# Kernel tuning notes

Hardware: AMD Instinct MI355X
Metric: run time of the kernel (lower is better)

The kernel has to match this reference:

```python
import jax, jax.numpy as jnp
import numpy as np

N_NODES = 50000
N_EDGES = 800000
IN_CH = 128
OUT_CH = 64


def setup_inputs() -> dict:
    key = jax.random.key(0)
    ks = jax.random.split(key, 8)
    cat = IN_CH + OUT_CH
    scale = 1.0 / np.sqrt(cat)
    return {
        "x": jax.random.normal(ks[0], (N_NODES, IN_CH), dtype=jnp.float32),
        "edge_index": jax.random.randint(ks[1], (2, N_EDGES), 0, N_NODES, dtype=jnp.int64),
        "edge_weight": jax.random.uniform(ks[2], (N_EDGES,), dtype=jnp.float32),
        "hidden_state": jax.random.normal(ks[3], (N_NODES, OUT_CH), dtype=jnp.float32),
        "W_z": jax.random.normal(ks[4], (cat, OUT_CH), dtype=jnp.float32) * scale,
        "b_z": jnp.zeros((OUT_CH,), dtype=jnp.float32),
        "W_r": jax.random.normal(ks[5], (cat, OUT_CH), dtype=jnp.float32) * scale,
        "b_r": jnp.zeros((OUT_CH,), dtype=jnp.float32),
        "W_h": jax.random.normal(ks[6], (cat, OUT_CH), dtype=jnp.float32) * scale,
        "b_h": jnp.zeros((OUT_CH,), dtype=jnp.float32),
    }


def _gcn_norm(row, col, w, num_nodes):
    # PyG GCNConv normalization with self-loops (fill_value=1):
    # norm_e = deg[row]^-1/2 * w_e * deg[col]^-1/2 over loop-augmented edges
    loops = jnp.arange(num_nodes, dtype=row.dtype)
    row = jnp.concatenate([row, loops])
    col = jnp.concatenate([col, loops])
    w = jnp.concatenate([w, jnp.ones((num_nodes,), dtype=w.dtype)])
    deg = jax.ops.segment_sum(w, col, num_segments=num_nodes)
    dinv = jnp.where(deg > 0, jax.lax.rsqrt(deg), 0.0)
    norm = dinv[row] * w * dinv[col]
    return row, col, norm


def _gcn_conv(x_cat, W, b, row, col, norm, num_nodes):
    h = x_cat @ W                                   # (N, out)
    msg = h[row] * norm[:, None]                    # (E+N, out) gather + scale
    out = jax.ops.segment_sum(msg, col, num_segments=num_nodes)
    return out + b


def reference(x, edge_index, edge_weight, hidden_state,
              W_z, b_z, W_r, b_r, W_h, b_h):
    n = x.shape[0]
    row, col, norm = _gcn_norm(edge_index[0], edge_index[1], edge_weight, n)
    xh = jnp.concatenate([x, hidden_state], axis=1)
    z = jax.nn.sigmoid(_gcn_conv(xh, W_z, b_z, row, col, norm, n))
    r = jax.nn.sigmoid(_gcn_conv(xh, W_r, b_r, row, col, norm, n))
    xrh = jnp.concatenate([x, r * hidden_state], axis=1)
    h_cand = jnp.tanh(_gcn_conv(xrh, W_h, b_h, row, col, norm, n))
    return z * hidden_state + (1.0 - z) * h_cand
```

## Files before the change

kernel.cpp:

```cpp
#include <hip/hip_runtime.h>
#include <hip/hip_bf16.h>
#include <cstdint>
#include <cstddef>

#define IN_CH   128
#define OUT_CH  64
#define CAT_CH  192

typedef short bf16x8 __attribute__((ext_vector_type(8)));
typedef float f32x4  __attribute__((ext_vector_type(4)));
typedef float f32x2  __attribute__((ext_vector_type(2)));
typedef unsigned long long u64;
typedef unsigned int u32;

__device__ __forceinline__ float sigmoidf_(float x) { return 1.f / (1.f + __expf(-x)); }

__device__ __forceinline__ unsigned short f2bf(float f) {
    u32 u = __float_as_uint(f);
    u32 r = (u + 0x7fffu + ((u >> 16) & 1u)) >> 16;
    return (unsigned short)r;
}
__device__ __forceinline__ float bflo(u32 v) { return __uint_as_float(v << 16); }
__device__ __forceinline__ float bfhi(u32 v) { return __uint_as_float(v & 0xffff0000u); }

__device__ __forceinline__ unsigned char f2e4m3(float f) {
    u32 p = __builtin_amdgcn_cvt_pk_fp8_f32(f, f, 0, false);
    return (unsigned char)p;
}
template <bool HI>
__device__ __forceinline__ f32x2 fp8pk(u32 v) {
    return __builtin_amdgcn_cvt_pk_f32_fp8((int)v, HI);
}

__global__ void detect_kernel(const unsigned int* __restrict__ ei, int* __restrict__ flag) {
    unsigned int v = ei[(threadIdx.x << 1) + 1];
    unsigned long long b = __ballot(v != 0u);
    if (threadIdx.x == 0) *flag = (b != 0ull) ? 1 : 0;
}

__device__ __forceinline__ int load_col(const void* ei, int i, int E, int f) {
    return f ? ((const int*)ei)[E + i] : (int)((const long long*)ei)[E + i];
}
__device__ __forceinline__ int load_row(const void* ei, int i, int E, int f) {
    return f ? ((const int*)ei)[i] : (int)((const long long*)ei)[i];
}

__global__ void hist2_kernel(const void* __restrict__ ei, const float* __restrict__ w,
                             u64* __restrict__ packed8, u32* __restrict__ rank,
                             const int* __restrict__ flag, int E, int N) {
    int i0 = (blockIdx.x * blockDim.x + threadIdx.x) * 2;
    if (i0 >= E) return;
    const u32 shard = blockIdx.x & 7;
    u64* __restrict__ shp = packed8 + (size_t)shard * N;
    int f = *flag;
    u32 rk[2];
#pragma unroll
    for (int k = 0; k < 2; k++) {
        int i = i0 + k;
        if (i < E) {
            int c = load_col(ei, i, E, f);
            u32 wq = __float2uint_rn(w[i] * 1048576.0f);
            u64 old = atomicAdd(&shp[c], (1ull << 32) | (u64)wq);
            rk[k] = (shard << 28) | (u32)(old >> 32);
        }
    }
#pragma unroll
    for (int k = 0; k < 2; k++)
        if (i0 + k < E) rank[i0 + k] = rk[k];
}

__global__ __launch_bounds__(256) void scan1_kernel(const u64* __restrict__ packed8,
                                                    float* __restrict__ dinv,
                                                    u32* __restrict__ shoff,
                                                    int* __restrict__ starts,
                                                    int* __restrict__ bsum, int n) {
    __shared__ int s[256];
    int i = blockIdx.x * 256 + threadIdx.x;
    int v = 0;
    if (i < n) {
        u32 run = 0, wsum = 0;
#pragma unroll
        for (int sh = 0; sh < 8; sh++) {
            u64 p = packed8[(size_t)sh * n + i];
            shoff[(size_t)sh * n + i] = run;
            run  += (u32)(p >> 32);
            wsum += (u32)p;
        }
        float ws = (float)wsum * (1.0f / 1048576.0f);
        dinv[i] = rsqrtf(1.0f + ws);
        v = (int)run;
    }
    s[threadIdx.x] = v;
    __syncthreads();
#pragma unroll
    for (int d = 1; d < 256; d <<= 1) {
        int t = (threadIdx.x >= d) ? s[threadIdx.x - d] : 0;
        __syncthreads();
        s[threadIdx.x] += t;
        __syncthreads();
    }
    if (i < n) starts[i] = s[threadIdx.x] - v;
    if (threadIdx.x == 255) bsum[blockIdx.x] = s[255];
}

__global__ __launch_bounds__(256) void scan2_kernel(int* __restrict__ bsum, int nb) {
    __shared__ int s[256];
    int t = threadIdx.x;
    int v = (t < nb) ? bsum[t] : 0;
    s[t] = v;
    __syncthreads();
#pragma unroll
    for (int d = 1; d < 256; d <<= 1) {
        int u = (t >= d) ? s[t - d] : 0;
        __syncthreads();
        s[t] += u;
        __syncthreads();
    }
    if (t < nb) bsum[t] = s[t] - v;
}

__global__ void scan3_kernel(int* __restrict__ starts, const int* __restrict__ boff,
                             int n, int E) {
    int i = blockIdx.x * blockDim.x + threadIdx.x;
    if (i == 0) starts[n] = E;
    if (i < n) starts[i] += boff[blockIdx.x];
}

__global__ void scatter2_kernel(const void* __restrict__ ei, const float* __restrict__ w,
                                const float* __restrict__ dinv, const int* __restrict__ starts,
                                const u32* __restrict__ shoff, const u32* __restrict__ rank,
                                u64* __restrict__ pairs, const int* __restrict__ flag,
                                int E, int N) {
    int i0 = (blockIdx.x * blockDim.x + threadIdx.x) * 4;
    if (i0 >= E) return;
    int f = *flag;
    int r[4], c[4];
#pragma unroll
    for (int k = 0; k < 4; k++) {
        int i = i0 + k;
        if (i < E) { r[k] = load_row(ei, i, E, f); c[k] = load_col(ei, i, E, f); }
    }
#pragma unroll
    for (int k = 0; k < 4; k++) {
        int i = i0 + k;
        if (i < E) {
            float nm = dinv[r[k]] * w[i] * dinv[c[k]];
            u32 rk = rank[i];
            u32 sh = rk >> 28, rks = rk & 0x0fffffffu;
            int pos = starts[c[k]] + (int)shoff[(size_t)sh * N + c[k]] + (int)rks;
            pairs[pos] = ((u64)__float_as_uint(nm) << 32) | (u32)(r[k] << 7);
        }
    }
}

__global__ void cvt_kernel(const float* __restrict__ x, const float* __restrict__ hidden,
                           unsigned short* __restrict__ xb, unsigned short* __restrict__ hb,
                           int nx, int nh) {
    int i4 = (blockIdx.x * blockDim.x + threadIdx.x) * 4;
    if (i4 < nx) {
        float4 v = *(const float4*)&x[i4];
        ushort4 o = { f2bf(v.x), f2bf(v.y), f2bf(v.z), f2bf(v.w) };
        *(ushort4*)&xb[i4] = o;
    } else {
        int j = i4 - nx;
        if (j < nh) {
            float4 v = *(const float4*)&hidden[j];
            ushort4 o = { f2bf(v.x), f2bf(v.y), f2bf(v.z), f2bf(v.w) };
            *(ushort4*)&hb[j] = o;
        }
    }
}

__global__ void packW_kernel(const float* __restrict__ Wz, const float* __restrict__ Wr,
                             const float* __restrict__ Wh,
                             unsigned short* __restrict__ Bzrt, unsigned short* __restrict__ Wht) {
    int i = blockIdx.x * blockDim.x + threadIdx.x;
    if (i >= 192 * CAT_CH) return;
    int col = i / CAT_CH, k = i % CAT_CH;
    if (col < 128) {
        float v = (col < 64) ? Wz[k * 64 + col] : Wr[k * 64 + (col - 64)];
        Bzrt[col * CAT_CH + k] = f2bf(v);
    } else {
        Wht[(col - 128) * CAT_CH + k] = f2bf(Wh[k * 64 + (col - 128)]);
    }
}

template <int TN, bool FP8OUT>
__global__ __launch_bounds__(256) void gemm_bf16_kernel(
    const unsigned short* __restrict__ A0, int a0w,
    const unsigned short* __restrict__ A1, int a1w,
    const unsigned short* __restrict__ Bt,
    void* __restrict__ Cout, int nrows)
{
    __shared__ unsigned short As[128][48];
    __shared__ unsigned short Bs[TN][200];

    const int t = threadIdx.x, lane = t & 63, wave = t >> 6;
    const int rowBase = blockIdx.x * 128;

    for (int idx = t * 8; idx < TN * CAT_CH; idx += 256 * 8) {
        int col = idx / CAT_CH, k = idx % CAT_CH;
        *(int4*)&Bs[col][k] = *(const int4*)&Bt[idx];
    }

    f32x4 acc[2][TN / 16];
#pragma unroll
    for (int rf = 0; rf < 2; rf++)
#pragma unroll
        for (int cf = 0; cf < TN / 16; cf++) acc[rf][cf] = (f32x4){0.f, 0.f, 0.f, 0.f};

    const int srow = t >> 1, half = t & 1;
    int arow = rowBase + srow;
    if (arow >= nrows) arow = nrows - 1;

    for (int k0 = 0; k0 < CAT_CH; k0 += 32) {
        __syncthreads();
        {
            const unsigned short* src = (k0 < a0w)
                ? A0 + (size_t)arow * a0w + k0
                : A1 + (size_t)arow * a1w + (k0 - a0w);
            *(int4*)&As[srow][half * 16] = *(const int4*)(src + half * 16);
            *(int4*)&As[srow][half * 16 + 8] = *(const int4*)(src + half * 16 + 8);
        }
        __syncthreads();

        const int rbase = wave * 32;
        const int koff = (lane >> 4) * 8;
        bf16x8 a0 = *(const bf16x8*)&As[rbase + (lane & 15)][koff];
        bf16x8 a1 = *(const bf16x8*)&As[rbase + 16 + (lane & 15)][koff];
#pragma unroll
        for (int cf = 0; cf < TN / 16; cf++) {
            bf16x8 b = *(const bf16x8*)&Bs[cf * 16 + (lane & 15)][k0 + koff];
            acc[0][cf] = __builtin_amdgcn_mfma_f32_16x16x32_bf16(a0, b, acc[0][cf], 0, 0, 0);
            acc[1][cf] = __builtin_amdgcn_mfma_f32_16x16x32_bf16(a1, b, acc[1][cf], 0, 0, 0);
        }
    }

#pragma unroll
    for (int rf = 0; rf < 2; rf++)
#pragma unroll
        for (int cf = 0; cf < TN / 16; cf++) {
            int row0 = rowBase + wave * 32 + rf * 16 + (lane >> 4) * 4;
            int col  = cf * 16 + (lane & 15);
#pragma unroll
            for (int r = 0; r < 4; r++) {
                int row = row0 + r;
                if (row < nrows) {
                    if (FP8OUT)
                        ((unsigned char*)Cout)[(size_t)row * TN + col] = f2e4m3(acc[rf][cf][r]);
                    else
                        ((unsigned short*)Cout)[(size_t)row * TN + col] = f2bf(acc[rf][cf][r]);
                }
            }
        }
}

__global__ __launch_bounds__(256) void spmm_zr_kernel(
    const unsigned char* __restrict__ H8, const u64* __restrict__ pairs,
    const int* __restrict__ starts, const float* __restrict__ dinv,
    const float* __restrict__ hidden, const float* __restrict__ bz,
    const float* __restrict__ br, float* __restrict__ Z,
    unsigned short* __restrict__ RHb, int N)
{
    int node = (blockIdx.x * 256 + threadIdx.x) >> 6;
    if (node >= N) return;
    const int lane = threadIdx.x & 63;
    const int sub = lane & 31, half = lane >> 5;
    int s = starts[node], e = starts[node + 1];
    float d = dinv[node], d2 = d * d;

    float a0 = 0.f, a1 = 0.f, a2 = 0.f, a3 = 0.f;
    if (half == 0) {
        u32 sv = *(const u32*)&H8[(size_t)node * 128 + sub * 4];
        f32x2 s01 = fp8pk<false>(sv), s23 = fp8pk<true>(sv);
        a0 = s01.x * d2; a1 = s01.y * d2; a2 = s23.x * d2; a3 = s23.y * d2;
    }

    int j = s;
    int full = s + ((e - s) & ~15);
    for (; j < full; j += 16) {
        u32 hv[8]; float nm[8];
#pragma unroll
        for (int k = 0; k < 8; k++) {
            u64 p = pairs[j + k * 2 + half];
            nm[k] = __uint_as_float((u32)(p >> 32));
            hv[k] = *(const u32*)&H8[(size_t)(u32)p + sub * 4];
        }
#pragma unroll
        for (int k = 0; k < 8; k++) {
            f32x2 h01 = fp8pk<false>(hv[k]), h23 = fp8pk<true>(hv[k]);
            a0 = fmaf(h01.x, nm[k], a0); a1 = fmaf(h01.y, nm[k], a1);
            a2 = fmaf(h23.x, nm[k], a2); a3 = fmaf(h23.y, nm[k], a3);
        }
    }
    if (j < e) {
        u32 hv[8]; float nm[8];
#pragma unroll
        for (int k = 0; k < 8; k++) {
            int jj = j + k * 2 + half;
            u64 p = pairs[(jj < e) ? jj : (e - 1)];
            nm[k] = (jj < e) ? __uint_as_float((u32)(p >> 32)) : 0.f;
            hv[k] = *(const u32*)&H8[(size_t)(u32)p + sub * 4];
        }
#pragma unroll
        for (int k = 0; k < 8; k++) {
            f32x2 h01 = fp8pk<false>(hv[k]), h23 = fp8pk<true>(hv[k]);
            a0 = fmaf(h01.x, nm[k], a0); a1 = fmaf(h01.y, nm[k], a1);
            a2 = fmaf(h23.x, nm[k], a2); a3 = fmaf(h23.y, nm[k], a3);
        }
    }

    a0 += __shfl_xor(a0, 32, 64);
    a1 += __shfl_xor(a1, 32, 64);
    a2 += __shfl_xor(a2, 32, 64);
    a3 += __shfl_xor(a3, 32, 64);

    if (half == 0) {
        if (sub < 16) {
            int c = sub * 4;
            float4 b4 = *(const float4*)&bz[c];
            float4 o = { sigmoidf_(a0 + b4.x), sigmoidf_(a1 + b4.y),
                         sigmoidf_(a2 + b4.z), sigmoidf_(a3 + b4.w) };
            *(float4*)&Z[(size_t)node * 64 + c] = o;
        } else {
            int c = (sub - 16) * 4;
            float4 b4 = *(const float4*)&br[c];
            float4 hid = *(const float4*)&hidden[(size_t)node * 64 + c];
            float r0 = sigmoidf_(a0 + b4.x) * hid.x;
            float r1 = sigmoidf_(a1 + b4.y) * hid.y;
            float r2 = sigmoidf_(a2 + b4.z) * hid.z;
            float r3 = sigmoidf_(a3 + b4.w) * hid.w;
            ushort4 o = { f2bf(r0), f2bf(r1), f2bf(r2), f2bf(r3) };
            *(ushort4*)&RHb[(size_t)node * 64 + c] = o;
        }
    }
}

__global__ __launch_bounds__(256) void spmm_h_kernel(
    const unsigned short* __restrict__ H, const u64* __restrict__ pairs,
    const int* __restrict__ starts, const float* __restrict__ dinv,
    const float* __restrict__ hidden, const float* __restrict__ bh,
    const float* __restrict__ Z, float* __restrict__ out, int N)
{
    int node = (blockIdx.x * 256 + threadIdx.x) >> 6;
    if (node >= N) return;
    const int lane = threadIdx.x & 63;
    const int sub = lane & 31, half = lane >> 5;
    const unsigned char* Hb = (const unsigned char*)H;
    int s = starts[node], e = starts[node + 1];
    float d = dinv[node], d2 = d * d;

    float ax = 0.f, ay = 0.f;
    if (half == 0) {
        u32 sv = *(const u32*)&Hb[(size_t)node * 128 + sub * 4];
        ax = bflo(sv) * d2; ay = bfhi(sv) * d2;
    }

    int j = s;
    int full = s + ((e - s) & ~15);
    for (; j < full; j += 16) {
        u32 hv[8]; float nm[8];
#pragma unroll
        for (int k = 0; k < 8; k++) {
            u64 p = pairs[j + k * 2 + half];
            nm[k] = __uint_as_float((u32)(p >> 32));
            hv[k] = *(const u32*)&Hb[(size_t)(u32)p + sub * 4];
        }
#pragma unroll
        for (int k = 0; k < 8; k++) {
            ax = fmaf(bflo(hv[k]), nm[k], ax);
            ay = fmaf(bfhi(hv[k]), nm[k], ay);
        }
    }
    if (j < e) {
        u32 hv[8]; float nm[8];
#pragma unroll
        for (int k = 0; k < 8; k++) {
            int jj = j + k * 2 + half;
            u64 p = pairs[(jj < e) ? jj : (e - 1)];
            nm[k] = (jj < e) ? __uint_as_float((u32)(p >> 32)) : 0.f;
            hv[k] = *(const u32*)&Hb[(size_t)(u32)p + sub * 4];
        }
#pragma unroll
        for (int k = 0; k < 8; k++) {
            ax = fmaf(bflo(hv[k]), nm[k], ax);
            ay = fmaf(bfhi(hv[k]), nm[k], ay);
        }
    }

    ax += __shfl_xor(ax, 32, 64);
    ay += __shfl_xor(ay, 32, 64);

    if (half == 0) {
        int c = sub * 2;
        size_t idx = (size_t)node * 64 + c;
        float2 hid = *(const float2*)&hidden[idx];
        float2 z   = *(const float2*)&Z[idx];
        float hc0 = tanhf(ax + bh[c]);
        float hc1 = tanhf(ay + bh[c + 1]);
        float2 o = { z.x * hid.x + (1.f - z.x) * hc0,
                     z.y * hid.y + (1.f - z.y) * hc1 };
        *(float2*)&out[idx] = o;
    }
}

extern "C" void kernel_launch(void* const* d_in, const int* in_sizes, int n_in,
                              void* d_out, int out_size, void* d_ws, size_t ws_size,
                              hipStream_t stream) {
    const float* x      = (const float*)d_in[0];
    const void*  eidx   = d_in[1];
    const float* ew     = (const float*)d_in[2];
    const float* hidden = (const float*)d_in[3];
    const float* Wz     = (const float*)d_in[4];
    const float* bz     = (const float*)d_in[5];
    const float* Wr     = (const float*)d_in[6];
    const float* br     = (const float*)d_in[7];
    const float* Wh     = (const float*)d_in[8];
    const float* bh     = (const float*)d_in[9];
    float* out = (float*)d_out;

    const int E = in_sizes[2];
    const int N = in_sizes[3] / OUT_CH;

    char* base = (char*)d_ws;
    size_t off = 0;
    auto carve = [&](size_t bytes) -> char* {
        char* p = base + off;
        off = (off + bytes + 255) & ~(size_t)255;
        return p;
    };
    u64*   packed8 = (u64*) carve((size_t)N * 8 * 8);
    u32*   shoff   = (u32*) carve((size_t)N * 8 * 4);
    u32*   rank    = (u32*) carve((size_t)E * 4);
    float* dinv    = (float*)carve((size_t)N * 4);
    int*   starts  = (int*)  carve((size_t)(N + 1) * 4);
    int*   bsum    = (int*)  carve(256 * 4);
    u64*   pairs   = (u64*)  carve((size_t)E * 8);
    unsigned short* xb   = (unsigned short*)carve((size_t)N * 128 * 2);
    unsigned short* hb   = (unsigned short*)carve((size_t)N * 64 * 2);
    unsigned char*  Hzr8 = (unsigned char*)carve((size_t)N * 128);
    unsigned short* RHb  = (unsigned short*)carve((size_t)N * 64 * 2);
    unsigned short* Hhb  = (unsigned short*)carve((size_t)N * 64 * 2);
    float* Z = (float*)carve((size_t)N * 64 * 4);
    unsigned short* Bzrt = (unsigned short*)carve((size_t)128 * CAT_CH * 2);
    unsigned short* Wht  = (unsigned short*)carve((size_t)64 * CAT_CH * 2);
    int* flag = (int*)carve(4);
    if (off > ws_size) return;

    const int B256 = 256;
    const int gE2 = (E + 511) / 512;
    const int gE4 = (E + 1023) / 1024;
    const int gN = (N + B256 - 1) / B256;
    const int gM = (N + 127) / 128;
    const int gW = (N + 3) / 4;

    hipLaunchKernelGGL(detect_kernel, dim3(1), dim3(64), 0, stream,
                       (const unsigned int*)eidx, flag);

    (void)hipMemsetAsync(packed8, 0, (size_t)N * 8 * 8, stream);
    hipLaunchKernelGGL(hist2_kernel, dim3(gE2), dim3(B256), 0, stream,
                       eidx, ew, packed8, rank, flag, E, N);

    hipLaunchKernelGGL(scan1_kernel, dim3(gN), dim3(B256), 0, stream,
                       packed8, dinv, shoff, starts, bsum, N);
    hipLaunchKernelGGL(scan2_kernel, dim3(1), dim3(B256), 0, stream, bsum, gN);
    hipLaunchKernelGGL(scan3_kernel, dim3(gN), dim3(B256), 0, stream, starts, bsum, N, E);

    hipLaunchKernelGGL(scatter2_kernel, dim3(gE4), dim3(B256), 0, stream,
                       eidx, ew, dinv, starts, shoff, rank, pairs, flag, E, N);

    hipLaunchKernelGGL(cvt_kernel, dim3((N * CAT_CH / 4 + 255) / 256), dim3(B256), 0, stream,
                       x, hidden, xb, hb, N * 128, N * 64);
    hipLaunchKernelGGL(packW_kernel, dim3((192 * CAT_CH + 255) / 256), dim3(B256), 0, stream,
                       Wz, Wr, Wh, Bzrt, Wht);

    hipLaunchKernelGGL((gemm_bf16_kernel<128, true>), dim3(gM), dim3(B256), 0, stream,
                       xb, 128, hb, 64, Bzrt, (void*)Hzr8, N);

    hipLaunchKernelGGL(spmm_zr_kernel, dim3(gW), dim3(B256), 0, stream,
                       Hzr8, pairs, starts, dinv, hidden, bz, br, Z, RHb, N);

    hipLaunchKernelGGL((gemm_bf16_kernel<64, false>), dim3(gM), dim3(B256), 0, stream,
                       xb, 128, RHb, 64, Wht, (void*)Hhb, N);

    hipLaunchKernelGGL(spmm_h_kernel, dim3(gW), dim3(B256), 0, stream,
                       Hhb, pairs, starts, dinv, hidden, bh, Z, out, N);
}
```

Measured before the change: 179.7 us.

## Fuse fp32-to-bf16 conversion into GEMM loads and merge prep kernels

```diff
diff --git a/kernel.cpp b/kernel.cpp
--- a/kernel.cpp
+++ b/kernel.cpp
@@ -20,6 +20,9 @@
     u32 r = (u + 0x7fffu + ((u >> 16) & 1u)) >> 16;
     return (unsigned short)r;
 }
+__device__ __forceinline__ u32 pk2bf(float a, float b) {
+    return (u32)f2bf(a) | ((u32)f2bf(b) << 16);
+}
 __device__ __forceinline__ float bflo(u32 v) { return __uint_as_float(v << 16); }
 __device__ __forceinline__ float bfhi(u32 v) { return __uint_as_float(v & 0xffff0000u); }
 
@@ -32,17 +35,41 @@
     return __builtin_amdgcn_cvt_pk_f32_fp8((int)v, HI);
 }
 
-__global__ void detect_kernel(const unsigned int* __restrict__ ei, int* __restrict__ flag) {
-    unsigned int v = ei[(threadIdx.x << 1) + 1];
-    unsigned long long b = __ballot(v != 0u);
-    if (threadIdx.x == 0) *flag = (b != 0ull) ? 1 : 0;
-}
-
 __device__ __forceinline__ int load_col(const void* ei, int i, int E, int f) {
     return f ? ((const int*)ei)[E + i] : (int)((const long long*)ei)[E + i];
 }
 __device__ __forceinline__ int load_row(const void* ei, int i, int E, int f) {
     return f ? ((const int*)ei)[i] : (int)((const long long*)ei)[i];
+}
+
+__global__ void prep_kernel(int4* __restrict__ zdst, int n16,
+                            const unsigned int* __restrict__ ei, int* __restrict__ flag,
+                            const float* __restrict__ Wz, const float* __restrict__ Wr,
+                            const float* __restrict__ Wh,
+                            unsigned short* __restrict__ Bzrt, unsigned short* __restrict__ Wht,
+                            int gZ) {
+    int b = blockIdx.x, t = threadIdx.x;
+    if (b < gZ) {
+        int i = b * 256 + t;
+        if (i < n16) zdst[i] = make_int4(0, 0, 0, 0);
+    } else if (b == gZ) {
+        if (t < 64) {
+            unsigned int v = ei[(t << 1) + 1];
+            unsigned long long bl = __ballot(v != 0u);
+            if (t == 0) *flag = (bl != 0ull) ? 1 : 0;
+        }
+    } else {
+        int i = (b - gZ - 1) * 256 + t;
+        if (i < 192 * CAT_CH) {
+            int col = i / CAT_CH, k = i % CAT_CH;
+            if (col < 128) {
+                float v = (col < 64) ? Wz[k * 64 + col] : Wr[k * 64 + (col - 64)];
+                Bzrt[col * CAT_CH + k] = f2bf(v);
+            } else {
+                Wht[(col - 128) * CAT_CH + k] = f2bf(Wh[k * 64 + (col - 128)]);
+            }
+        }
+    }
 }
 
 __global__ void hist2_kernel(const void* __restrict__ ei, const float* __restrict__ w,
@@ -153,42 +180,10 @@
     }
 }
 
-__global__ void cvt_kernel(const float* __restrict__ x, const float* __restrict__ hidden,
-                           unsigned short* __restrict__ xb, unsigned short* __restrict__ hb,
-                           int nx, int nh) {
-    int i4 = (blockIdx.x * blockDim.x + threadIdx.x) * 4;
-    if (i4 < nx) {
-        float4 v = *(const float4*)&x[i4];
-        ushort4 o = { f2bf(v.x), f2bf(v.y), f2bf(v.z), f2bf(v.w) };
-        *(ushort4*)&xb[i4] = o;
-    } else {
-        int j = i4 - nx;
-        if (j < nh) {
-            float4 v = *(const float4*)&hidden[j];
-            ushort4 o = { f2bf(v.x), f2bf(v.y), f2bf(v.z), f2bf(v.w) };
-            *(ushort4*)&hb[j] = o;
-        }
-    }
-}
-
-__global__ void packW_kernel(const float* __restrict__ Wz, const float* __restrict__ Wr,
-                             const float* __restrict__ Wh,
-                             unsigned short* __restrict__ Bzrt, unsigned short* __restrict__ Wht) {
-    int i = blockIdx.x * blockDim.x + threadIdx.x;
-    if (i >= 192 * CAT_CH) return;
-    int col = i / CAT_CH, k = i % CAT_CH;
-    if (col < 128) {
-        float v = (col < 64) ? Wz[k * 64 + col] : Wr[k * 64 + (col - 64)];
-        Bzrt[col * CAT_CH + k] = f2bf(v);
-    } else {
-        Wht[(col - 128) * CAT_CH + k] = f2bf(Wh[k * 64 + (col - 128)]);
-    }
-}
-
-template <int TN, bool FP8OUT>
+template <int TN, bool FP8OUT, bool A1F32>
 __global__ __launch_bounds__(256) void gemm_bf16_kernel(
-    const unsigned short* __restrict__ A0, int a0w,
-    const unsigned short* __restrict__ A1, int a1w,
+    const float* __restrict__ A0, int a0w,
+    const void* __restrict__ A1, int a1w,
     const unsigned short* __restrict__ Bt,
     void* __restrict__ Cout, int nrows)
 {
@@ -216,11 +211,34 @@
     for (int k0 = 0; k0 < CAT_CH; k0 += 32) {
         __syncthreads();
         {
-            const unsigned short* src = (k0 < a0w)
-                ? A0 + (size_t)arow * a0w + k0
-                : A1 + (size_t)arow * a1w + (k0 - a0w);
-            *(int4*)&As[srow][half * 16] = *(const int4*)(src + half * 16);
-            *(int4*)&As[srow][half * 16 + 8] = *(const int4*)(src + half * 16 + 8);
+            int kk = k0 + half * 16;
+            u32 pk[8];
+            if (kk < a0w) {
+                const float* src = A0 + (size_t)arow * a0w + kk;
+#pragma unroll
+                for (int q = 0; q < 4; q++) {
+                    float4 v = *(const float4*)(src + q * 4);
+                    pk[q * 2]     = pk2bf(v.x, v.y);
+                    pk[q * 2 + 1] = pk2bf(v.z, v.w);
+                }
+            } else if (A1F32) {
+                const float* src = (const float*)A1 + (size_t)arow * a1w + (kk - a0w);
+#pragma unroll
+                for (int q = 0; q < 4; q++) {
+                    float4 v = *(const float4*)(src + q * 4);
+                    pk[q * 2]     = pk2bf(v.x, v.y);
+                    pk[q * 2 + 1] = pk2bf(v.z, v.w);
+                }
+            } else {
+                const unsigned short* src =
+                    (const unsigned short*)A1 + (size_t)arow * a1w + (kk - a0w);
+                int4 v0 = *(const int4*)src;
+                int4 v1 = *(const int4*)(src + 8);
+                pk[0] = v0.x; pk[1] = v0.y; pk[2] = v0.z; pk[3] = v0.w;
+                pk[4] = v1.x; pk[5] = v1.y; pk[6] = v1.z; pk[7] = v1.w;
+            }
+            *(int4*)&As[srow][half * 16]     = make_int4(pk[0], pk[1], pk[2], pk[3]);
+            *(int4*)&As[srow][half * 16 + 8] = make_int4(pk[4], pk[5], pk[6], pk[7]);
         }
         __syncthreads();
 
@@ -436,8 +454,6 @@
     int*   starts  = (int*)  carve((size_t)(N + 1) * 4);
     int*   bsum    = (int*)  carve(256 * 4);
     u64*   pairs   = (u64*)  carve((size_t)E * 8);
-    unsigned short* xb   = (unsigned short*)carve((size_t)N * 128 * 2);
-    unsigned short* hb   = (unsigned short*)carve((size_t)N * 64 * 2);
     unsigned char*  Hzr8 = (unsigned char*)carve((size_t)N * 128);
     unsigned short* RHb  = (unsigned short*)carve((size_t)N * 64 * 2);
     unsigned short* Hhb  = (unsigned short*)carve((size_t)N * 64 * 2);
@@ -453,11 +469,14 @@
     const int gN = (N + B256 - 1) / B256;
     const int gM = (N + 127) / 128;
     const int gW = (N + 3) / 4;
-
-    hipLaunchKernelGGL(detect_kernel, dim3(1), dim3(64), 0, stream,
-                       (const unsigned int*)eidx, flag);
-
-    (void)hipMemsetAsync(packed8, 0, (size_t)N * 8 * 8, stream);
+    const int n16 = N * 4;
+    const int gZ = (n16 + B256 - 1) / B256;
+    const int gP = (192 * CAT_CH + 255) / 256;
+
+    hipLaunchKernelGGL(prep_kernel, dim3(gZ + 1 + gP), dim3(B256), 0, stream,
+                       (int4*)packed8, n16, (const unsigned int*)eidx, flag,
+                       Wz, Wr, Wh, Bzrt, Wht, gZ);
+
     hipLaunchKernelGGL(hist2_kernel, dim3(gE2), dim3(B256), 0, stream,
                        eidx, ew, packed8, rank, flag, E, N);
 
@@ -469,19 +488,14 @@
     hipLaunchKernelGGL(scatter2_kernel, dim3(gE4), dim3(B256), 0, stream,
                        eidx, ew, dinv, starts, shoff, rank, pairs, flag, E, N);
 
-    hipLaunchKernelGGL(cvt_kernel, dim3((N * CAT_CH / 4 + 255) / 256), dim3(B256), 0, stream,
-                       x, hidden, xb, hb, N * 128, N * 64);
-    hipLaunchKernelGGL(packW_kernel, dim3((192 * CAT_CH + 255) / 256), dim3(B256), 0, stream,
-                       Wz, Wr, Wh, Bzrt, Wht);
-
-    hipLaunchKernelGGL((gemm_bf16_kernel<128, true>), dim3(gM), dim3(B256), 0, stream,
-                       xb, 128, hb, 64, Bzrt, (void*)Hzr8, N);
+    hipLaunchKernelGGL((gemm_bf16_kernel<128, true, true>), dim3(gM), dim3(B256), 0, stream,
+                       x, 128, (const void*)hidden, 64, Bzrt, (void*)Hzr8, N);
 
     hipLaunchKernelGGL(spmm_zr_kernel, dim3(gW), dim3(B256), 0, stream,
                        Hzr8, pairs, starts, dinv, hidden, bz, br, Z, RHb, N);
 
-    hipLaunchKernelGGL((gemm_bf16_kernel<64, false>), dim3(gM), dim3(B256), 0, stream,
-                       xb, 128, RHb, 64, Wht, (void*)Hhb, N);
+    hipLaunchKernelGGL((gemm_bf16_kernel<64, false, false>), dim3(gM), dim3(B256), 0, stream,
+                       x, 128, (const void*)RHb, 64, Wht, (void*)Hhb, N);
 
     hipLaunchKernelGGL(spmm_h_kernel, dim3(gW), dim3(B256), 0, stream,
                        Hhb, pairs, starts, dinv, hidden, bh, Z, out, N);
```

Result: faster. 169.9 us (-5.5%).
